# Kernel optimization log

Hardware: AMD Instinct MI355X
Metric: run time of the kernel (lower is better)

The kernel has to match this reference:

```python
import jax, jax.numpy as jnp
import numpy as np

N_NODES = 100000
N_EDGES = 3200000
IN_DIM, HID, OUT_DIM = 128, 64, 32
N_LAYERS = 3


def setup_inputs() -> dict:
    key = jax.random.key(0)
    ks = jax.random.split(key, 10)
    x = jax.random.normal(ks[0], (N_NODES, IN_DIM), dtype=jnp.float32)
    edge_index = jax.random.randint(ks[1], (2, N_EDGES), 0, N_NODES, dtype=jnp.int64)
    edge_weight = jax.random.uniform(ks[2], (N_EDGES,), dtype=jnp.float32)
    s_in = 1.0 / np.sqrt(IN_DIM)
    s_h = 1.0 / np.sqrt(HID)
    W_in = jax.random.uniform(ks[3], (IN_DIM, HID), jnp.float32, -s_in, s_in)
    b_in = jax.random.uniform(ks[4], (HID,), jnp.float32, -s_in, s_in)
    W_g = jax.random.uniform(ks[5], (N_LAYERS, HID, HID), jnp.float32, -s_h, s_h)
    b_g = jax.random.uniform(ks[6], (N_LAYERS, HID), jnp.float32, -s_h, s_h)
    W_out = jax.random.uniform(ks[7], (HID, OUT_DIM), jnp.float32, -s_h, s_h)
    b_out = jax.random.uniform(ks[8], (OUT_DIM,), jnp.float32, -s_h, s_h)
    return {"x": x, "edge_index": edge_index, "edge_weight": edge_weight,
            "W_in": W_in, "b_in": b_in, "W_g": W_g, "b_g": b_g,
            "W_out": W_out, "b_out": b_out}


def reference(x, edge_index, edge_weight, W_in, b_in, W_g, b_g, W_out, b_out):
    # input projection: [N, IN_DIM] -> [N, HID]
    h = x @ W_in + b_in
    src = edge_index[0]
    dst = edge_index[1]
    num_nodes = h.shape[0]
    for l in range(N_LAYERS):
        # per-edge message: gather source features, scale by edge weight
        msg = h[src] * edge_weight[:, None]          # [E, HID]
        agg = jax.ops.segment_sum(msg, dst, num_segments=num_nodes)  # [N, HID]
        h = jax.nn.relu((h + agg) @ W_g[l] + b_g[l])
    return h @ W_out + b_out
```

## Files before the change

kernel.cpp:

```cpp
#include <hip/hip_runtime.h>
#include <hip/hip_bf16.h>
#include <hip/hip_fp16.h>

#define N_NODES 100000
#define IN_DIM 128
#define HID 64
#define OUT_DIM 32
#define BUCK 128
#define NB 782
#define CAP 5120
#define AST 68
#define CHUNK 8192

typedef float floatx2 __attribute__((ext_vector_type(2)));
typedef short bf16x8 __attribute__((ext_vector_type(8)));
typedef float f32x4 __attribute__((ext_vector_type(4)));

__device__ __forceinline__ unsigned int pack4_fp8(float f0, float f1, float f2, float f3) {
    int u = __builtin_amdgcn_cvt_pk_fp8_f32(f0, f1, 0, false);
    u     = __builtin_amdgcn_cvt_pk_fp8_f32(f2, f3, u, true);
    return (unsigned int)u;
}

__device__ __forceinline__ unsigned short f2bf(float f) {
    unsigned int u = __float_as_uint(f);
    return (unsigned short)((u + 0x7FFFu + ((u >> 16) & 1u)) >> 16);
}

__global__ __launch_bounds__(512) void k_part(const int* __restrict__ src,
                                              const int* __restrict__ dst,
                                              const float* __restrict__ ew,
                                              int* __restrict__ bcur,
                                              unsigned int* __restrict__ ed, int E) {
    __shared__ int cnt[NB];
    __shared__ int lscan[NB];
    __shared__ int base[NB];
    __shared__ unsigned int stage[CHUNK];
    const int tid = threadIdx.x;
    const int lo = blockIdx.x * CHUNK;
    const int hi = min(E, lo + CHUNK);

    for (int i = tid; i < NB; i += 512) cnt[i] = 0;
    __syncthreads();
    for (int e = lo + tid; e < hi; e += 512)
        atomicAdd(&cnt[dst[e] >> 7], 1);
    __syncthreads();
    {
        const int i0 = tid, i1 = tid + 512;
        if (i0 < NB) lscan[i0] = cnt[i0];
        if (i1 < NB) lscan[i1] = cnt[i1];
        __syncthreads();
        for (int d = 1; d < 1024; d <<= 1) {
            int v0 = 0, v1 = 0;
            if (i0 >= d && i0 < NB) v0 = lscan[i0 - d];
            if (i1 >= d && i1 < NB) v1 = lscan[i1 - d];
            __syncthreads();
            if (i0 < NB) lscan[i0] += v0;
            if (i1 < NB) lscan[i1] += v1;
            __syncthreads();
        }
    }
    for (int i = tid; i < NB; i += 512) {
        int c = cnt[i];
        lscan[i] -= c;
        base[i] = c ? atomicAdd(&bcur[i], c) : 0;
        cnt[i] = 0;
    }
    __syncthreads();
    for (int e = lo + tid; e < hi; e += 512) {
        int d  = dst[e];
        int bk = d >> 7;
        unsigned int q = (unsigned int)(ew[e] * 256.0f);
        if (q > 255u) q = 255u;
        int r = atomicAdd(&cnt[bk], 1);
        stage[lscan[bk] + r] = (unsigned int)src[e]
                               | ((unsigned int)(d & 127) << 17) | (q << 24);
    }
    __syncthreads();
    for (int b = tid; b < NB; b += 512) {
        int c = cnt[b];
        if (!c) continue;
        int room = CAP - base[b];
        int m = c < room ? c : (room > 0 ? room : 0);
        const unsigned int* s = &stage[lscan[b]];
        unsigned int* g = ed + (size_t)b * CAP + base[b];
        for (int i = 0; i < m; ++i) g[i] = s[i];
    }
}

__global__ __launch_bounds__(512) void k_sort(const unsigned int* __restrict__ ed,
                                              unsigned int* __restrict__ ed2,
                                              const int* __restrict__ bcur,
                                              int* __restrict__ off,
                                              int* __restrict__ endo) {
    __shared__ int cnt[BUCK];
    __shared__ int inc[BUCK];
    __shared__ int cur[BUCK];
    const int tid = threadIdx.x;
    const int bkt = blockIdx.x;
    const int b0 = bkt * CAP;
    const int b1 = b0 + min(bcur[bkt], CAP);

    if (tid < BUCK) cnt[tid] = 0;
    __syncthreads();
    for (int i = b0 + tid; i < b1; i += 512)
        atomicAdd(&cnt[(ed[i] >> 17) & 127], 1);
    __syncthreads();
    if (tid < BUCK) inc[tid] = cnt[tid];
    __syncthreads();
    for (int d = 1; d < BUCK; d <<= 1) {
        int v = 0;
        if (tid < BUCK && tid >= d) v = inc[tid - d];
        __syncthreads();
        if (tid < BUCK) inc[tid] += v;
        __syncthreads();
    }
    if (tid < BUCK) {
        int ex = inc[tid] - cnt[tid];
        cur[tid] = ex;
        int n = bkt * BUCK + tid;
        if (n < N_NODES) {
            off[n]  = b0 + ex;
            endo[n] = b0 + ex + cnt[tid];
        }
    }
    __syncthreads();
    for (int i = b0 + tid; i < b1; i += 512) {
        unsigned int e = ed[i];
        int dl = (e >> 17) & 127;
        int p = atomicAdd(&cur[dl], 1);
        ed2[b0 + p] = e;
    }
}

__global__ __launch_bounds__(256) void k_wc(const float* __restrict__ W_in,
                                            const float* __restrict__ b_in,
                                            const float* __restrict__ Wg0,
                                            unsigned short* __restrict__ wct,
                                            float* __restrict__ bc) {
    __shared__ float sWg[HID * HID];
    __shared__ float sWi[16 * HID];
    const int tid = threadIdx.x;
    const int k0 = blockIdx.x * 16;
    for (int i = tid; i < HID * HID; i += 256) sWg[i] = Wg0[i];
    for (int i = tid; i < 16 * HID; i += 256) sWi[i] = W_in[k0 * HID + i];
    __syncthreads();
    const int kr = tid >> 4;
    const int jb = (tid & 15) * 4;
    float c0 = 0.f, c1 = 0.f, c2 = 0.f, c3 = 0.f;
#pragma unroll 4
    for (int m = 0; m < HID; ++m) {
        const float a = sWi[kr * HID + m];
        const float4 wv = *(const float4*)&sWg[m * HID + jb];
        c0 = fmaf(a, wv.x, c0); c1 = fmaf(a, wv.y, c1);
        c2 = fmaf(a, wv.z, c2); c3 = fmaf(a, wv.w, c3);
    }
    const int k = k0 + kr;
    wct[(size_t)(jb + 0) * IN_DIM + k] = f2bf(c0);
    wct[(size_t)(jb + 1) * IN_DIM + k] = f2bf(c1);
    wct[(size_t)(jb + 2) * IN_DIM + k] = f2bf(c2);
    wct[(size_t)(jb + 3) * IN_DIM + k] = f2bf(c3);
    if (blockIdx.x == 0 && tid < HID) {
        float s = 0.f;
        for (int m = 0; m < HID; ++m) s = fmaf(b_in[m], sWg[m * HID + tid], s);
        bc[tid] = s;
    }
}

__global__ __launch_bounds__(256) void k_proj0(const float* __restrict__ x,
                                               const unsigned short* __restrict__ wct,
                                               const float* __restrict__ bc,
                                               unsigned int* __restrict__ g0) {
    __shared__ float sH[4][32][76];
    const int tid = threadIdx.x;
    const int w = tid >> 6, lane = tid & 63;
    const int lr = lane & 15, lg = lane >> 4;
    const int nb0 = blockIdx.x * 128 + w * 32;

    bf16x8 B[4][4];
#pragma unroll
    for (int j = 0; j < 4; ++j)
#pragma unroll
        for (int c = 0; c < 4; ++c)
            B[j][c] = *(const bf16x8*)(wct + (16 * j + lr) * IN_DIM + 32 * c + 8 * lg);

    f32x4 acc[2][4];
#pragma unroll
    for (int mt = 0; mt < 2; ++mt)
#pragma unroll
        for (int j = 0; j < 4; ++j)
            acc[mt][j] = (f32x4){0.f, 0.f, 0.f, 0.f};

#pragma unroll
    for (int mt = 0; mt < 2; ++mt) {
        int n = nb0 + mt * 16 + lr;
        if (n >= N_NODES) n = N_NODES - 1;
        const float* xr = x + (size_t)n * IN_DIM + 8 * lg;
        bf16x8 A[4];
#pragma unroll
        for (int c = 0; c < 4; ++c) {
            const float4 lo = *(const float4*)(xr + 32 * c);
            const float4 hi = *(const float4*)(xr + 32 * c + 4);
            bf16x8 a;
            a[0] = (short)f2bf(lo.x); a[1] = (short)f2bf(lo.y);
            a[2] = (short)f2bf(lo.z); a[3] = (short)f2bf(lo.w);
            a[4] = (short)f2bf(hi.x); a[5] = (short)f2bf(hi.y);
            a[6] = (short)f2bf(hi.z); a[7] = (short)f2bf(hi.w);
            A[c] = a;
        }
#pragma unroll
        for (int j = 0; j < 4; ++j)
#pragma unroll
            for (int c = 0; c < 4; ++c)
                acc[mt][j] = __builtin_amdgcn_mfma_f32_16x16x32_bf16(
                    A[c], B[j][c], acc[mt][j], 0, 0, 0);
    }

#pragma unroll
    for (int j = 0; j < 4; ++j) {
        const float bj = bc[16 * j + lr];
#pragma unroll
        for (int mt = 0; mt < 2; ++mt)
#pragma unroll
            for (int r = 0; r < 4; ++r)
                sH[w][mt * 16 + 4 * lg + r][16 * j + lr] = acc[mt][j][r] + bj;
    }
    __syncthreads();

#pragma unroll
    for (int i = 0; i < 8; ++i) {
        const int idx = lane + 64 * i;
        const int nl = idx >> 4, jq = idx & 15;
        const int n = nb0 + nl;
        if (n < N_NODES) {
            const float4 v = *(const float4*)&sH[w][nl][jq * 4];
            g0[(size_t)n * 16 + jq] = pack4_fp8(v.x, v.y, v.z, v.w);
        }
    }
}

#define ROW(p)  (gp[((size_t)((p) & 0x1FFFFu)) * 8])
#define WT(p)   (((float)((p) >> 24) + 0.5f) * 0.00390625f)
#define ACC(p, v) do { const float w_ = WT(p); const floatx2 w2 = {w_, w_};     \
        A01 += w2 * __builtin_amdgcn_cvt_pk_f32_fp8((v).x, false);              \
        A23 += w2 * __builtin_amdgcn_cvt_pk_f32_fp8((v).x, true);               \
        A45 += w2 * __builtin_amdgcn_cvt_pk_f32_fp8((v).y, false);              \
        A67 += w2 * __builtin_amdgcn_cvt_pk_f32_fp8((v).y, true); } while (0)

#define AGG_GATHER_BODY                                                        \
    floatx2 A01 = {0.f, 0.f}, A23 = {0.f, 0.f},                                \
            A45 = {0.f, 0.f}, A67 = {0.f, 0.f};                                \
    if (valid) {                                                               \
        uint2 sv = gp[(size_t)n * 8];                                          \
        A01 = __builtin_amdgcn_cvt_pk_f32_fp8(sv.x, false);                    \
        A23 = __builtin_amdgcn_cvt_pk_f32_fp8(sv.x, true);                     \
        A45 = __builtin_amdgcn_cvt_pk_f32_fp8(sv.y, false);                    \
        A67 = __builtin_amdgcn_cvt_pk_f32_fp8(sv.y, true);                     \
        int i = off[n];                                                        \
        const int i1 = endo[n];                                                \
        if (i + 4 <= i1) {                                                     \
            unsigned int p0 = ed2[i], p1 = ed2[i+1], p2 = ed2[i+2], p3 = ed2[i+3]; \
            uint2 v0 = ROW(p0), v1 = ROW(p1), v2 = ROW(p2), v3 = ROW(p3);      \
            i += 4;                                                            \
            for (; i + 4 <= i1; i += 4) {                                      \
                unsigned int q0 = ed2[i], q1 = ed2[i+1], q2 = ed2[i+2], q3 = ed2[i+3]; \
                uint2 w0 = ROW(q0), w1 = ROW(q1), w2 = ROW(q2), w3 = ROW(q3);  \
                ACC(p0, v0); ACC(p1, v1); ACC(p2, v2); ACC(p3, v3);            \
                p0 = q0; p1 = q1; p2 = q2; p3 = q3;                            \
                v0 = w0; v1 = w1; v2 = w2; v3 = w3;                            \
            }                                                                  \
            ACC(p0, v0); ACC(p1, v1); ACC(p2, v2); ACC(p3, v3);                \
        }                                                                      \
        for (; i < i1; ++i) { unsigned int p = ed2[i]; uint2 v = ROW(p); ACC(p, v); } \
    }                                                                          \
    const float a0 = A01.x, a1 = A01.y, a2 = A23.x, a3 = A23.y,                \
                a4 = A45.x, a5 = A45.y, a6 = A67.x, a7 = A67.y;

__global__ __launch_bounds__(512) void k_agg_mid(
        const unsigned int* __restrict__ g_in,
        unsigned int* __restrict__ g_out,
        const unsigned int* __restrict__ ed2,
        const int* __restrict__ off, const int* __restrict__ endo,
        const float* __restrict__ bg, const float* __restrict__ Wnext) {
    __shared__ float sHT[HID][AST];
    __shared__ float sW[HID * HID];
    const int tid = threadIdx.x;
    const int grp = tid >> 3, l8 = tid & 7;
    const int n = blockIdx.x * 64 + grp;
    const bool valid = (n < N_NODES);
    const uint2* gp = (const uint2*)g_in + l8;

    for (int i = tid; i < HID * HID; i += 512) sW[i] = Wnext[i];

    AGG_GATHER_BODY

    const float4 bA = *(const float4*)(bg + l8 * 8);
    const float4 bB = *(const float4*)(bg + l8 * 8 + 4);
    const int f0 = l8 * 8;
    sHT[f0 + 0][grp] = valid ? fmaxf(a0 + bA.x, 0.f) : 0.f;
    sHT[f0 + 1][grp] = valid ? fmaxf(a1 + bA.y, 0.f) : 0.f;
    sHT[f0 + 2][grp] = valid ? fmaxf(a2 + bA.z, 0.f) : 0.f;
    sHT[f0 + 3][grp] = valid ? fmaxf(a3 + bA.w, 0.f) : 0.f;
    sHT[f0 + 4][grp] = valid ? fmaxf(a4 + bB.x, 0.f) : 0.f;
    sHT[f0 + 5][grp] = valid ? fmaxf(a5 + bB.y, 0.f) : 0.f;
    sHT[f0 + 6][grp] = valid ? fmaxf(a6 + bB.z, 0.f) : 0.f;
    sHT[f0 + 7][grp] = valid ? fmaxf(a7 + bB.w, 0.f) : 0.f;
    __syncthreads();

    const int npr = tid >> 4;
    const int jq  = tid & 15;
    const int jb  = jq * 4;
    float c0[4] = {0.f, 0.f, 0.f, 0.f};
    float c1[4] = {0.f, 0.f, 0.f, 0.f};
#pragma unroll 4
    for (int k = 0; k < HID; ++k) {
        const float2 a = *(const float2*)&sHT[k][npr * 2];
        const float4 w = *(const float4*)&sW[k * HID + jb];
        c0[0] = fmaf(a.x, w.x, c0[0]); c0[1] = fmaf(a.x, w.y, c0[1]);
        c0[2] = fmaf(a.x, w.z, c0[2]); c0[3] = fmaf(a.x, w.w, c0[3]);
        c1[0] = fmaf(a.y, w.x, c1[0]); c1[1] = fmaf(a.y, w.y, c1[1]);
        c1[2] = fmaf(a.y, w.z, c1[2]); c1[3] = fmaf(a.y, w.w, c1[3]);
    }
    const int nbase = blockIdx.x * 64 + npr * 2;
    if (nbase < N_NODES)
        g_out[(size_t)nbase * 16 + jq] = pack4_fp8(c0[0], c0[1], c0[2], c0[3]);
    if (nbase + 1 < N_NODES)
        g_out[(size_t)(nbase + 1) * 16 + jq] = pack4_fp8(c1[0], c1[1], c1[2], c1[3]);
}

__global__ __launch_bounds__(512) void k_agg_out(
        const unsigned int* __restrict__ g_in,
        float* __restrict__ out,
        const unsigned int* __restrict__ ed2,
        const int* __restrict__ off, const int* __restrict__ endo,
        const float* __restrict__ bg, const float* __restrict__ W_out,
        const float* __restrict__ b_out) {
    __shared__ float sHT[HID][AST];
    __shared__ float sW[HID * OUT_DIM];
    const int tid = threadIdx.x;
    const int grp = tid >> 3, l8 = tid & 7;
    const int n = blockIdx.x * 64 + grp;
    const bool valid = (n < N_NODES);
    const uint2* gp = (const uint2*)g_in + l8;

    for (int i = tid; i < HID * OUT_DIM; i += 512) sW[i] = W_out[i];

    AGG_GATHER_BODY

    const float4 bA = *(const float4*)(bg + l8 * 8);
    const float4 bB = *(const float4*)(bg + l8 * 8 + 4);
    const int f0 = l8 * 8;
    sHT[f0 + 0][grp] = valid ? fmaxf(a0 + bA.x, 0.f) : 0.f;
    sHT[f0 + 1][grp] = valid ? fmaxf(a1 + bA.y, 0.f) : 0.f;
    sHT[f0 + 2][grp] = valid ? fmaxf(a2 + bA.z, 0.f) : 0.f;
    sHT[f0 + 3][grp] = valid ? fmaxf(a3 + bA.w, 0.f) : 0.f;
    sHT[f0 + 4][grp] = valid ? fmaxf(a4 + bB.x, 0.f) : 0.f;
    sHT[f0 + 5][grp] = valid ? fmaxf(a5 + bB.y, 0.f) : 0.f;
    sHT[f0 + 6][grp] = valid ? fmaxf(a6 + bB.z, 0.f) : 0.f;
    sHT[f0 + 7][grp] = valid ? fmaxf(a7 + bB.w, 0.f) : 0.f;
    __syncthreads();

    const int node = tid >> 3;
    const int jb   = (tid & 7) * 4;
    const float4 bo = *(const float4*)(b_out + jb);
    float c4[4] = {bo.x, bo.y, bo.z, bo.w};
#pragma unroll 4
    for (int k = 0; k < HID; ++k) {
        const float a = sHT[k][node];
        const float4 w = *(const float4*)&sW[k * OUT_DIM + jb];
        c4[0] = fmaf(a, w.x, c4[0]); c4[1] = fmaf(a, w.y, c4[1]);
        c4[2] = fmaf(a, w.z, c4[2]); c4[3] = fmaf(a, w.w, c4[3]);
    }
    const int n2 = blockIdx.x * 64 + node;
    if (n2 < N_NODES)
        *(float4*)(out + (size_t)n2 * OUT_DIM + jb) =
            make_float4(c4[0], c4[1], c4[2], c4[3]);
}

#undef ROW
#undef WT
#undef ACC
#undef AGG_GATHER_BODY

extern "C" void kernel_launch(void* const* d_in, const int* in_sizes, int n_in,
                              void* d_out, int out_size, void* d_ws, size_t ws_size,
                              hipStream_t stream) {
    const float* x     = (const float*)d_in[0];
    const int*   ei    = (const int*)d_in[1];
    const float* ew    = (const float*)d_in[2];
    const float* W_in  = (const float*)d_in[3];
    const float* b_in  = (const float*)d_in[4];
    const float* W_g   = (const float*)d_in[5];
    const float* b_g   = (const float*)d_in[6];
    const float* W_out = (const float*)d_in[7];
    const float* b_out = (const float*)d_in[8];
    float* out = (float*)d_out;

    const int E = in_sizes[2];
    const int* src = ei;
    const int* dst = ei + E;

    char* ws = (char*)d_ws;
    unsigned int* ed  = (unsigned int*)ws;
    unsigned int* ed2 = ed + (size_t)NB * CAP;
    unsigned int* gA  = ed2 + (size_t)NB * CAP;
    unsigned int* gB  = gA + (size_t)N_NODES * 16;
    int* misc = (int*)(gB + (size_t)N_NODES * 16);
    int* off  = misc;
    int* endo = misc + 100032;
    int* bcur = misc + 200064;

    const int nparts = (E + CHUNK - 1) / CHUNK;

    unsigned short* wct = (unsigned short*)ed;
    float* bcv = (float*)(ed + 4096);

    k_wc<<<8, 256, 0, stream>>>(W_in, b_in, W_g, wct, bcv);
    k_proj0<<<(N_NODES + 127) / 128, 256, 0, stream>>>(x, wct, bcv, gA);

    hipMemsetAsync(bcur, 0, NB * sizeof(int), stream);
    k_part<<<nparts, 512, 0, stream>>>(src, dst, ew, bcur, ed, E);
    k_sort<<<NB, 512, 0, stream>>>(ed, ed2, bcur, off, endo);

    k_agg_mid<<<(N_NODES + 63) / 64, 512, 0, stream>>>(
        gA, gB, ed2, off, endo, b_g + 0 * HID, W_g + 1 * HID * HID);
    k_agg_mid<<<(N_NODES + 63) / 64, 512, 0, stream>>>(
        gB, gA, ed2, off, endo, b_g + 1 * HID, W_g + 2 * HID * HID);
    k_agg_out<<<(N_NODES + 63) / 64, 512, 0, stream>>>(
        gA, out, ed2, off, endo, b_g + 2 * HID, W_out, b_out);
}
```

Measured before the change: 348.7 us.

## Stage per-block edge records in LDS and deepen gather prefetch pipeline

Each aggregation block now cooperatively loads the contiguous range of packed edge records for its 64 nodes into shared memory with nontemporal loads, so each 8-lane group reads its records from LDS instead of issuing redundant global loads. The gather loop is deepened to keep 8 row loads in flight, and a 3-wide tail replaces the scalar remainder loop. In k_agg_mid, the weight matrix is no longer staged in shared memory and is read from global/cache during the matmul, which frees LDS for the records. The cost is an extra barrier before the gather and more register pressure. Blocks whose record range exceeds the capacity fall back to the global path.

```diff
diff --git a/kernel.cpp b/kernel.cpp
--- a/kernel.cpp
+++ b/kernel.cpp
@@ -11,6 +11,7 @@
 #define CAP 5120
 #define AST 68
 #define CHUNK 8192
+#define RECCAP 3072
 
 typedef float floatx2 __attribute__((ext_vector_type(2)));
 typedef short bf16x8 __attribute__((ext_vector_type(8)));
@@ -241,11 +242,21 @@
 
 #define ROW(p)  (gp[((size_t)((p) & 0x1FFFFu)) * 8])
 #define WT(p)   (((float)((p) >> 24) + 0.5f) * 0.00390625f)
+#define REC(i)  stage[(i) - rbase]
 #define ACC(p, v) do { const float w_ = WT(p); const floatx2 w2 = {w_, w_};     \
         A01 += w2 * __builtin_amdgcn_cvt_pk_f32_fp8((v).x, false);              \
         A23 += w2 * __builtin_amdgcn_cvt_pk_f32_fp8((v).x, true);               \
         A45 += w2 * __builtin_amdgcn_cvt_pk_f32_fp8((v).y, false);              \
         A67 += w2 * __builtin_amdgcn_cvt_pk_f32_fp8((v).y, true); } while (0)
+
+#define AGG_STAGE_RECORDS                                                      \
+    const int n0b   = blockIdx.x * 64;                                         \
+    const int nlast = min(n0b + 63, N_NODES - 1);                              \
+    const int rbase = off[n0b];                                                \
+    const int rcnt  = min(endo[nlast] - rbase, RECCAP);                        \
+    for (int idx = tid; idx < rcnt; idx += 512)                                \
+        stage[idx] = __builtin_nontemporal_load(ed2 + rbase + idx);            \
+    __syncthreads();
 
 #define AGG_GATHER_BODY                                                        \
     floatx2 A01 = {0.f, 0.f}, A23 = {0.f, 0.f},                                \
@@ -258,20 +269,51 @@
         A67 = __builtin_amdgcn_cvt_pk_f32_fp8(sv.y, true);                     \
         int i = off[n];                                                        \
         const int i1 = endo[n];                                                \
-        if (i + 4 <= i1) {                                                     \
-            unsigned int p0 = ed2[i], p1 = ed2[i+1], p2 = ed2[i+2], p3 = ed2[i+3]; \
-            uint2 v0 = ROW(p0), v1 = ROW(p1), v2 = ROW(p2), v3 = ROW(p3);      \
-            i += 4;                                                            \
-            for (; i + 4 <= i1; i += 4) {                                      \
-                unsigned int q0 = ed2[i], q1 = ed2[i+1], q2 = ed2[i+2], q3 = ed2[i+3]; \
-                uint2 w0 = ROW(q0), w1 = ROW(q1), w2 = ROW(q2), w3 = ROW(q3);  \
+        if (i1 - rbase <= RECCAP) {    \
+            if (i + 8 <= i1) {                                                 \
+                unsigned int p0 = REC(i),   p1 = REC(i+1);                     \
+                unsigned int p2 = REC(i+2), p3 = REC(i+3);                     \
+                unsigned int p4 = REC(i+4), p5 = REC(i+5);                     \
+                unsigned int p6 = REC(i+6), p7 = REC(i+7);                     \
+                uint2 v0 = ROW(p0), v1 = ROW(p1), v2 = ROW(p2), v3 = ROW(p3);  \
+                uint2 v4 = ROW(p4), v5 = ROW(p5), v6 = ROW(p6), v7 = ROW(p7);  \
+                i += 8;                                                        \
+                _Pragma("unroll 2")                                            \
+                for (; i + 4 <= i1; i += 4) {                                  \
+                    unsigned int q0 = REC(i),   q1 = REC(i+1);                 \
+                    unsigned int q2 = REC(i+2), q3 = REC(i+3);                 \
+                    uint2 w0 = ROW(q0), w1 = ROW(q1);                          \
+                    uint2 w2 = ROW(q2), w3 = ROW(q3);                          \
+                    ACC(p0, v0); ACC(p1, v1); ACC(p2, v2); ACC(p3, v3);        \
+                    p0 = p4; p1 = p5; p2 = p6; p3 = p7;                        \
+                    v0 = v4; v1 = v5; v2 = v6; v3 = v7;                        \
+                    p4 = q0; p5 = q1; p6 = q2; p7 = q3;                        \
+                    v4 = w0; v5 = w1; v6 = w2; v7 = w3;                        \
+                }                                                              \
                 ACC(p0, v0); ACC(p1, v1); ACC(p2, v2); ACC(p3, v3);            \
-                p0 = q0; p1 = q1; p2 = q2; p3 = q3;                            \
-                v0 = w0; v1 = w1; v2 = w2; v3 = w3;                            \
+                ACC(p4, v4); ACC(p5, v5); ACC(p6, v6); ACC(p7, v7);            \
+            } else if (i + 4 <= i1) {                                          \
+                unsigned int p0 = REC(i),   p1 = REC(i+1);                     \
+                unsigned int p2 = REC(i+2), p3 = REC(i+3);                     \
+                uint2 v0 = ROW(p0), v1 = ROW(p1), v2 = ROW(p2), v3 = ROW(p3);  \
+                i += 4;                                                        \
+                ACC(p0, v0); ACC(p1, v1); ACC(p2, v2); ACC(p3, v3);            \
             }                                                                  \
-            ACC(p0, v0); ACC(p1, v1); ACC(p2, v2); ACC(p3, v3);                \
+            const int r = i1 - i;                                              \
+            if (r > 0) {                                                       \
+                unsigned int t0 = REC(i);                                      \
+                unsigned int t1 = REC(i + (r > 1 ? 1 : 0));                    \
+                unsigned int t2 = REC(i + (r > 2 ? 2 : 0));                    \
+                uint2 u0 = ROW(t0), u1 = ROW(t1), u2 = ROW(t2);                \
+                ACC(t0, u0);                                                   \
+                if (r > 1) ACC(t1, u1);                                        \
+                if (r > 2) ACC(t2, u2);                                        \
+            }                                                                  \
+        } else {                           \
+            for (; i < i1; ++i) {                                              \
+                unsigned int p = ed2[i]; uint2 v = ROW(p); ACC(p, v);          \
+            }                                                                  \
         }                                                                      \
-        for (; i < i1; ++i) { unsigned int p = ed2[i]; uint2 v = ROW(p); ACC(p, v); } \
     }                                                                          \
     const float a0 = A01.x, a1 = A01.y, a2 = A23.x, a3 = A23.y,                \
                 a4 = A45.x, a5 = A45.y, a6 = A67.x, a7 = A67.y;
@@ -283,14 +325,14 @@
         const int* __restrict__ off, const int* __restrict__ endo,
         const float* __restrict__ bg, const float* __restrict__ Wnext) {
     __shared__ float sHT[HID][AST];
-    __shared__ float sW[HID * HID];
+    __shared__ unsigned int stage[RECCAP];
     const int tid = threadIdx.x;
     const int grp = tid >> 3, l8 = tid & 7;
     const int n = blockIdx.x * 64 + grp;
     const bool valid = (n < N_NODES);
     const uint2* gp = (const uint2*)g_in + l8;
 
-    for (int i = tid; i < HID * HID; i += 512) sW[i] = Wnext[i];
+    AGG_STAGE_RECORDS
 
     AGG_GATHER_BODY
 
@@ -315,7 +357,7 @@
 #pragma unroll 4
     for (int k = 0; k < HID; ++k) {
         const float2 a = *(const float2*)&sHT[k][npr * 2];
-        const float4 w = *(const float4*)&sW[k * HID + jb];
+        const float4 w = *(const float4*)&Wnext[k * HID + jb];
         c0[0] = fmaf(a.x, w.x, c0[0]); c0[1] = fmaf(a.x, w.y, c0[1]);
         c0[2] = fmaf(a.x, w.z, c0[2]); c0[3] = fmaf(a.x, w.w, c0[3]);
         c1[0] = fmaf(a.y, w.x, c1[0]); c1[1] = fmaf(a.y, w.y, c1[1]);
@@ -337,6 +379,7 @@
         const float* __restrict__ b_out) {
     __shared__ float sHT[HID][AST];
     __shared__ float sW[HID * OUT_DIM];
+    __shared__ unsigned int stage[RECCAP];
     const int tid = threadIdx.x;
     const int grp = tid >> 3, l8 = tid & 7;
     const int n = blockIdx.x * 64 + grp;
@@ -344,6 +387,8 @@
     const uint2* gp = (const uint2*)g_in + l8;
 
     for (int i = tid; i < HID * OUT_DIM; i += 512) sW[i] = W_out[i];
+
+    AGG_STAGE_RECORDS
 
     AGG_GATHER_BODY
 
@@ -379,7 +424,9 @@
 
 #undef ROW
 #undef WT
+#undef REC
 #undef ACC
+#undef AGG_STAGE_RECORDS
 #undef AGG_GATHER_BODY
 
 extern "C" void kernel_launch(void* const* d_in, const int* in_sizes, int n_in,
```

Result: no change. 353.9 us (+1.5%).

## Replace bucket partition+local sort with global counting sort keyed by dst and src

Applied to the files above, without the earlier changes.

Replaces the two-pass bucket partition (LDS staging per chunk, then per-bucket local sort) with a global counting sort. A histogram over keys (dst*4 + two high bits of src) is followed by a three-kernel prefix scan and an atomic scatter into a CSR edge array. Sub-ordering each node's edges by src range is meant to improve gather locality in the three aggregation passes. It also removes the fixed bucket capacity and the separate end-offset array. The cost is heavier use of global atomics with returned values, a 400K-entry memset, and more kernel launches.

```diff
diff --git a/kernel.cpp b/kernel.cpp
--- a/kernel.cpp
+++ b/kernel.cpp
@@ -6,11 +6,10 @@
 #define IN_DIM 128
 #define HID 64
 #define OUT_DIM 32
-#define BUCK 128
-#define NB 782
-#define CAP 5120
 #define AST 68
-#define CHUNK 8192
+#define NKEY (N_NODES * 4)
+#define SCAN_TILE 4096
+#define NSB ((NKEY + SCAN_TILE - 1) / SCAN_TILE)
 
 typedef float floatx2 __attribute__((ext_vector_type(2)));
 typedef short bf16x8 __attribute__((ext_vector_type(8)));
@@ -27,109 +26,95 @@
     return (unsigned short)((u + 0x7FFFu + ((u >> 16) & 1u)) >> 16);
 }
 
-__global__ __launch_bounds__(512) void k_part(const int* __restrict__ src,
+__global__ __launch_bounds__(512) void k_hist(const int* __restrict__ src,
                                               const int* __restrict__ dst,
-                                              const float* __restrict__ ew,
-                                              int* __restrict__ bcur,
-                                              unsigned int* __restrict__ ed, int E) {
-    __shared__ int cnt[NB];
-    __shared__ int lscan[NB];
-    __shared__ int base[NB];
-    __shared__ unsigned int stage[CHUNK];
-    const int tid = threadIdx.x;
-    const int lo = blockIdx.x * CHUNK;
-    const int hi = min(E, lo + CHUNK);
-
-    for (int i = tid; i < NB; i += 512) cnt[i] = 0;
-    __syncthreads();
-    for (int e = lo + tid; e < hi; e += 512)
-        atomicAdd(&cnt[dst[e] >> 7], 1);
-    __syncthreads();
-    {
-        const int i0 = tid, i1 = tid + 512;
-        if (i0 < NB) lscan[i0] = cnt[i0];
-        if (i1 < NB) lscan[i1] = cnt[i1];
+                                              int* __restrict__ cnt, int E) {
+    const int t = blockIdx.x * 512 + threadIdx.x;
+    const int stride = gridDim.x * 512;
+    for (int e = t; e < E; e += stride) {
+        const int d = dst[e], s = src[e];
+        atomicAdd(&cnt[(d << 2) | ((s >> 15) & 3)], 1);
+    }
+}
+
+__global__ __launch_bounds__(512) void k_scan1(const int* __restrict__ cnt,
+                                               int* __restrict__ S,
+                                               int* __restrict__ bsum) {
+    __shared__ int tsum[512];
+    const int tid = threadIdx.x;
+    const int base = blockIdx.x * SCAN_TILE + tid * 8;
+    int v[8]; int s = 0;
+#pragma unroll
+    for (int j = 0; j < 8; ++j) {
+        const int idx = base + j;
+        v[j] = (idx < NKEY) ? cnt[idx] : 0;
+        s += v[j];
+    }
+    tsum[tid] = s; __syncthreads();
+    for (int d = 1; d < 512; d <<= 1) {
+        int tv = (tid >= d) ? tsum[tid - d] : 0;
         __syncthreads();
-        for (int d = 1; d < 1024; d <<= 1) {
-            int v0 = 0, v1 = 0;
-            if (i0 >= d && i0 < NB) v0 = lscan[i0 - d];
-            if (i1 >= d && i1 < NB) v1 = lscan[i1 - d];
-            __syncthreads();
-            if (i0 < NB) lscan[i0] += v0;
-            if (i1 < NB) lscan[i1] += v1;
-            __syncthreads();
+        tsum[tid] += tv;
+        __syncthreads();
+    }
+    int run = tsum[tid] - s;
+#pragma unroll
+    for (int j = 0; j < 8; ++j) {
+        const int idx = base + j;
+        if (idx < NKEY) S[idx] = run;
+        run += v[j];
+    }
+    if (tid == 511) bsum[blockIdx.x] = tsum[511];
+}
+
+__global__ __launch_bounds__(128) void k_scan2(const int* __restrict__ bsum,
+                                               int* __restrict__ bbase) {
+    __shared__ int b[128];
+    const int tid = threadIdx.x;
+    const int v = (tid < NSB) ? bsum[tid] : 0;
+    b[tid] = v; __syncthreads();
+    for (int d = 1; d < 128; d <<= 1) {
+        int tv = (tid >= d) ? b[tid - d] : 0;
+        __syncthreads();
+        b[tid] += tv;
+        __syncthreads();
+    }
+    if (tid < NSB) bbase[tid] = b[tid] - v;
+}
+
+__global__ __launch_bounds__(512) void k_scan3(int* __restrict__ S,
+                                               const int* __restrict__ bbase,
+                                               int* __restrict__ off, int E) {
+    const int tid = threadIdx.x;
+    const int bb = bbase[blockIdx.x];
+    const int base = blockIdx.x * SCAN_TILE;
+#pragma unroll
+    for (int j = 0; j < 8; ++j) {
+        const int idx = base + j * 512 + tid;
+        if (idx < NKEY) {
+            const int vv = S[idx] + bb;
+            S[idx] = vv;
+            if ((idx & 3) == 0) off[idx >> 2] = vv;
         }
     }
-    for (int i = tid; i < NB; i += 512) {
-        int c = cnt[i];
-        lscan[i] -= c;
-        base[i] = c ? atomicAdd(&bcur[i], c) : 0;
-        cnt[i] = 0;
-    }
-    __syncthreads();
-    for (int e = lo + tid; e < hi; e += 512) {
-        int d  = dst[e];
-        int bk = d >> 7;
+    if (blockIdx.x == 0 && tid == 0) off[N_NODES] = E;
+}
+
+__global__ __launch_bounds__(512) void k_scatter(const int* __restrict__ src,
+                                                 const int* __restrict__ dst,
+                                                 const float* __restrict__ ew,
+                                                 int* __restrict__ S,
+                                                 unsigned int* __restrict__ ed2,
+                                                 int E) {
+    const int t = blockIdx.x * 512 + threadIdx.x;
+    const int stride = gridDim.x * 512;
+    for (int e = t; e < E; e += stride) {
+        const int d = dst[e], s = src[e];
         unsigned int q = (unsigned int)(ew[e] * 256.0f);
         if (q > 255u) q = 255u;
-        int r = atomicAdd(&cnt[bk], 1);
-        stage[lscan[bk] + r] = (unsigned int)src[e]
-                               | ((unsigned int)(d & 127) << 17) | (q << 24);
-    }
-    __syncthreads();
-    for (int b = tid; b < NB; b += 512) {
-        int c = cnt[b];
-        if (!c) continue;
-        int room = CAP - base[b];
-        int m = c < room ? c : (room > 0 ? room : 0);
-        const unsigned int* s = &stage[lscan[b]];
-        unsigned int* g = ed + (size_t)b * CAP + base[b];
-        for (int i = 0; i < m; ++i) g[i] = s[i];
-    }
-}
-
-__global__ __launch_bounds__(512) void k_sort(const unsigned int* __restrict__ ed,
-                                              unsigned int* __restrict__ ed2,
-                                              const int* __restrict__ bcur,
-                                              int* __restrict__ off,
-                                              int* __restrict__ endo) {
-    __shared__ int cnt[BUCK];
-    __shared__ int inc[BUCK];
-    __shared__ int cur[BUCK];
-    const int tid = threadIdx.x;
-    const int bkt = blockIdx.x;
-    const int b0 = bkt * CAP;
-    const int b1 = b0 + min(bcur[bkt], CAP);
-
-    if (tid < BUCK) cnt[tid] = 0;
-    __syncthreads();
-    for (int i = b0 + tid; i < b1; i += 512)
-        atomicAdd(&cnt[(ed[i] >> 17) & 127], 1);
-    __syncthreads();
-    if (tid < BUCK) inc[tid] = cnt[tid];
-    __syncthreads();
-    for (int d = 1; d < BUCK; d <<= 1) {
-        int v = 0;
-        if (tid < BUCK && tid >= d) v = inc[tid - d];
-        __syncthreads();
-        if (tid < BUCK) inc[tid] += v;
-        __syncthreads();
-    }
-    if (tid < BUCK) {
-        int ex = inc[tid] - cnt[tid];
-        cur[tid] = ex;
-        int n = bkt * BUCK + tid;
-        if (n < N_NODES) {
-            off[n]  = b0 + ex;
-            endo[n] = b0 + ex + cnt[tid];
-        }
-    }
-    __syncthreads();
-    for (int i = b0 + tid; i < b1; i += 512) {
-        unsigned int e = ed[i];
-        int dl = (e >> 17) & 127;
-        int p = atomicAdd(&cur[dl], 1);
-        ed2[b0 + p] = e;
+        const int key = (d << 2) | ((s >> 15) & 3);
+        const int p = atomicAdd(&S[key], 1);
+        ed2[p] = (unsigned int)s | (q << 24);
     }
 }
 
@@ -399,33 +384,34 @@
     const int E = in_sizes[2];
     const int* src = ei;
     const int* dst = ei + E;
+    const int Epad = (E + 3) & ~3;
 
     char* ws = (char*)d_ws;
-    unsigned int* ed  = (unsigned int*)ws;
-    unsigned int* ed2 = ed + (size_t)NB * CAP;
-    unsigned int* gA  = ed2 + (size_t)NB * CAP;
+    unsigned int* ed2 = (unsigned int*)ws;
+    unsigned int* gA  = ed2 + (size_t)Epad;
     unsigned int* gB  = gA + (size_t)N_NODES * 16;
-    int* misc = (int*)(gB + (size_t)N_NODES * 16);
-    int* off  = misc;
-    int* endo = misc + 100032;
-    int* bcur = misc + 200064;
-
-    const int nparts = (E + CHUNK - 1) / CHUNK;
-
-    unsigned short* wct = (unsigned short*)ed;
-    float* bcv = (float*)(ed + 4096);
+    int* S    = (int*)(gB + (size_t)N_NODES * 16);
+    int* cnt  = S + NKEY;
+    int* off  = cnt + NKEY;
+    int* bsum = off + N_NODES + 4;
+    int* bbase = bsum + NSB;
+    unsigned short* wct = (unsigned short*)(bbase + NSB + 4);
+    float* bcv = (float*)(wct + IN_DIM * HID);
 
     k_wc<<<8, 256, 0, stream>>>(W_in, b_in, W_g, wct, bcv);
     k_proj0<<<(N_NODES + 127) / 128, 256, 0, stream>>>(x, wct, bcv, gA);
 
-    hipMemsetAsync(bcur, 0, NB * sizeof(int), stream);
-    k_part<<<nparts, 512, 0, stream>>>(src, dst, ew, bcur, ed, E);
-    k_sort<<<NB, 512, 0, stream>>>(ed, ed2, bcur, off, endo);
+    hipMemsetAsync(cnt, 0, NKEY * sizeof(int), stream);
+    k_hist<<<1024, 512, 0, stream>>>(src, dst, cnt, E);
+    k_scan1<<<NSB, 512, 0, stream>>>(cnt, S, bsum);
+    k_scan2<<<1, 128, 0, stream>>>(bsum, bbase);
+    k_scan3<<<NSB, 512, 0, stream>>>(S, bbase, off, E);
+    k_scatter<<<1024, 512, 0, stream>>>(src, dst, ew, S, ed2, E);
 
     k_agg_mid<<<(N_NODES + 63) / 64, 512, 0, stream>>>(
-        gA, gB, ed2, off, endo, b_g + 0 * HID, W_g + 1 * HID * HID);
+        gA, gB, ed2, off, off + 1, b_g + 0 * HID, W_g + 1 * HID * HID);
     k_agg_mid<<<(N_NODES + 63) / 64, 512, 0, stream>>>(
-        gB, gA, ed2, off, endo, b_g + 1 * HID, W_g + 2 * HID * HID);
+        gB, gA, ed2, off, off + 1, b_g + 1 * HID, W_g + 2 * HID * HID);
     k_agg_out<<<(N_NODES + 63) / 64, 512, 0, stream>>>(
-        gA, out, ed2, off, endo, b_g + 2 * HID, W_out, b_out);
-}
+        gA, out, ed2, off, off + 1, b_g + 2 * HID, W_out, b_out);
+}
```

After: 623.4 us. 78.8% more time.
